# Performance work log

Hardware: AMD Instinct MI355X
Metric: run time of the kernel (lower is better)

The kernel has to match this reference:

```python
import jax, jax.numpy as jnp
import numpy as np

N = 524288   # number of (column, layer) samples
NCH = 30     # n_channel, fixed by the hard-coded filter vectors

# Per-gas channel filters for (h2o, o3, co2, u, n2o, ch4), each length 30.
FILTERS = jnp.array([
    [1,1,1,1,1,1,1,1,1,1,1,1,1,1,1,1,1,1,1,1,1,1,0,0,0,0,0,0,1,1],  # h2o
    [1,1,0,0,0,0,0,0,0,0,0,0,0,0,0,0,1,1,1,1,1,1,0,0,1,1,1,1,1,1],  # o3
    [1,1,0,0,1,1,0,0,1,1,0,0,1,1,0,0,0,0,0,0,0,0,0,0,0,0,0,0,1,1],  # co2
    [1,1,0,0,0,0,0,0,0,0,0,0,0,0,1,1,1,1,1,1,1,1,0,0,0,0,1,1,1,1],  # u
    [1,1,0,0,1,0,0,0,0,0,0,0,0,0,0,0,0,0,0,0,0,0,0,0,0,0,0,0,1,1],  # n2o
    [1,1,1,1,0,0,1,1,0,0,1,1,0,0,0,0,0,0,0,0,0,0,0,0,0,0,0,0,1,1],  # ch4
], dtype=jnp.float32)


def setup_inputs() -> dict:
    key = jax.random.key(0)
    ks = jax.random.split(key, 11)
    u = lambda k, shape, lo, hi: jax.random.uniform(k, shape, jnp.float32, lo, hi)
    return {
        "tpl": jax.random.normal(ks[0], (N, 3), jnp.float32),   # temp, pressure, log_pressure
        "cons": jax.random.uniform(ks[1], (N, 8), jnp.float32), # constituent masses
        # eight Linear(1, 30, bias=False) weights (lw, iw, h2o, o3, co2, u, n2o, ch4)
        "w_gas": u(ks[2], (8, NCH), -0.9, 0.5),
        # six ke-MLPs (2 -> 6 -> 4 -> 4 -> 1), stacked over gas axis g=6
        "ke_W1": u(ks[3], (6, 6, 2), -0.1, 0.1),
        "ke_b1": u(ks[4], (6, 6), 0.9, 1.1),
        "ke_W2": u(ks[5], (6, 4, 6), -0.1, 0.1),
        "ke_b2": u(ks[6], (6, 4), 0.9, 1.1),
        "ke_W3": u(ks[7], (6, 4, 4), -0.1, 0.1),
        "ke_b3": u(ks[8], (6, 4), 0.9, 1.1),
        "ke_Wo": u(ks[9], (6, 4), -0.1, 0.1),
        "ke_bo": u(ks[10], (6,), -0.1, 0.1),
    }


def reference(tpl, cons, w_gas, ke_W1, ke_b1, ke_W2, ke_b2, ke_W3, ke_b3, ke_Wo, ke_bo):
    t_p = tpl[:, :2]                                             # [N,2]
    # six tiny MLPs, vectorized over gas axis g (dropout is identity at eval)
    h = jax.nn.relu(jnp.einsum('ghi,ni->gnh', ke_W1, t_p) + ke_b1[:, None, :])   # [6,N,6]
    h = jax.nn.relu(jnp.einsum('goh,gnh->gno', ke_W2, h) + ke_b2[:, None, :])    # [6,N,4]
    h = jax.nn.relu(jnp.einsum('gph,gnh->gnp', ke_W3, h) + ke_b3[:, None, :])    # [6,N,4]
    s = jax.nn.sigmoid(jnp.einsum('gp,gnp->gn', ke_Wo, h) + ke_bo[:, None])      # [6,N]

    # net_gas(one) == weight vector; exp(w_gas) gives per-channel extinction coeffs
    tau_base = cons[:, None, :] * jnp.exp(w_gas).T[None, :, :]                   # [N,30,8]
    # channel filter * sigmoid modulation for the 6 gas species (slots 2..7)
    mod_gas = (FILTERS[:, None, :] * s[:, :, None]).transpose(1, 2, 0)           # [N,30,6]
    mod = jnp.concatenate(
        [jnp.ones((tpl.shape[0], NCH, 2), tau_base.dtype), mod_gas], axis=2)     # [N,30,8]
    return tau_base * mod                                                        # [N,30,8]
```

## Files before the change

kernel.cpp:

```cpp
#include <hip/hip_runtime.h>

#define NCHAN 30

__constant__ int FMASK_C[NCHAN] = {63,63,33,33,21,5,33,33,5,5,33,33,5,5,9,9,
                                   11,11,11,11,11,11,0,0,2,2,10,10,63,63};

typedef float f32x4 __attribute__((ext_vector_type(4)));

__global__ __launch_bounds__(256) void ext_kernel(
    const float* __restrict__ tpl,
    const float* __restrict__ cons,
    const float* __restrict__ w_gas,
    const float* __restrict__ W1, const float* __restrict__ b1,
    const float* __restrict__ W2, const float* __restrict__ b2,
    const float* __restrict__ W3, const float* __restrict__ b3,
    const float* __restrict__ Wo, const float* __restrict__ bo,
    f32x4* __restrict__ out4)
{
    __shared__ float p_lds[256][8];
    __shared__ float E_lds[32][8];

    const int tid = threadIdx.x;
    const int n   = blockIdx.x * 256 + tid;

    if (tid < 8 * NCHAN) {
        const int c = tid >> 3, k = tid & 7;
        float e = __expf(w_gas[k * NCHAN + c]);
        if (k >= 2 && !((FMASK_C[c] >> (k - 2)) & 1)) e = 0.f;
        E_lds[c][k] = e;
    }

    const float4* c4 = (const float4*)cons;
    const float4 ca = c4[(size_t)n * 2];
    const float4 cb = c4[(size_t)n * 2 + 1];
    const float t0 = tpl[(size_t)n * 3 + 0];
    const float t1 = tpl[(size_t)n * 3 + 1];

    float s[6];
    #pragma unroll
    for (int g = 0; g < 6; ++g) {
        float h1[6], h2[4], h3[4];
        #pragma unroll
        for (int j = 0; j < 6; ++j)
            h1[j] = fmaxf(0.f, fmaf(W1[g*12 + j*2], t0,
                           fmaf(W1[g*12 + j*2 + 1], t1, b1[g*6 + j])));
        #pragma unroll
        for (int o = 0; o < 4; ++o) {
            float a = b2[g*4 + o];
            #pragma unroll
            for (int j = 0; j < 6; ++j) a = fmaf(W2[g*24 + o*6 + j], h1[j], a);
            h2[o] = fmaxf(0.f, a);
        }
        #pragma unroll
        for (int p = 0; p < 4; ++p) {
            float a = b3[g*4 + p];
            #pragma unroll
            for (int o = 0; o < 4; ++o) a = fmaf(W3[g*16 + p*4 + o], h2[o], a);
            h3[p] = fmaxf(0.f, a);
        }
        float a = bo[g];
        #pragma unroll
        for (int p = 0; p < 4; ++p) a = fmaf(Wo[g*4 + p], h3[p], a);
        s[g] = __fdividef(1.f, 1.f + __expf(-a));
    }

    float4 pa, pb;
    pa.x = ca.x;        pa.y = ca.y;
    pa.z = ca.z * s[0]; pa.w = ca.w * s[1];
    pb.x = cb.x * s[2]; pb.y = cb.y * s[3];
    pb.z = cb.z * s[4]; pb.w = cb.w * s[5];
    *(float4*)&p_lds[tid][0] = pa;
    *(float4*)&p_lds[tid][4] = pb;

    __syncthreads();

    const int lane = tid & 63;
    const int wid  = tid >> 6;

    const int erem = (lane < 60) ? lane : 0;
    const float4 ev = *(const float4*)&E_lds[erem >> 1][(erem & 1) << 2];
    const unsigned hi4 = (unsigned)(lane & 1) << 2;

    const size_t gbase = (size_t)blockIdx.x * (256 * NCHAN * 2);

    if (lane < 60) {
        const int r0 = wid * 64;
        #pragma unroll 4
        for (int r = 0; r < 64; ++r) {
            const int nl = r0 + r;
            const float4 pv = *(const float4*)&p_lds[nl][hi4];

            f32x4 v;
            v.x = pv.x * ev.x;
            v.y = pv.y * ev.y;
            v.z = pv.z * ev.z;
            v.w = pv.w * ev.w;
            __builtin_nontemporal_store(v, &out4[gbase + (size_t)nl * 60 + lane]);
        }
    }
}

extern "C" void kernel_launch(void* const* d_in, const int* in_sizes, int n_in,
                              void* d_out, int out_size, void* d_ws, size_t ws_size,
                              hipStream_t stream) {
    const float* tpl  = (const float*)d_in[0];
    const float* cons = (const float*)d_in[1];
    const float* wgas = (const float*)d_in[2];
    const float* W1   = (const float*)d_in[3];
    const float* b1   = (const float*)d_in[4];
    const float* W2   = (const float*)d_in[5];
    const float* b2   = (const float*)d_in[6];
    const float* W3   = (const float*)d_in[7];
    const float* b3   = (const float*)d_in[8];
    const float* Wo   = (const float*)d_in[9];
    const float* bo   = (const float*)d_in[10];

    const int nrows  = in_sizes[0] / 3;
    const int blocks = nrows / 256;

    ext_kernel<<<dim3(blocks), dim3(256), 0, stream>>>(
        tpl, cons, wgas, W1, b1, W2, b2, W3, b3, Wo, bo, (f32x4*)d_out);
}
```

Measured before the change: 103.4 us.

## Make each wave process four row tiles with prefetch and wave-local LDS staging

Each wave now handles four consecutive 64-row tiles in a loop, using a per-wave LDS slice and wave barriers instead of a block-wide __syncthreads. The next tile's inputs are prefetched while the current tile's outputs are stored. The per-channel exp table is computed directly in registers per lane, which removes the shared E table and its block sync. Grid size shrinks by a factor of four, so per-block setup such as the exp work is amortised. The cost is fewer blocks to hide memory latency in a store-bound kernel.

Result: slower. 110.0 us (+6.3%).

```diff
diff --git a/kernel.cpp b/kernel.cpp
--- a/kernel.cpp
+++ b/kernel.cpp
@@ -1,6 +1,7 @@
 #include <hip/hip_runtime.h>
 
 #define NCHAN 30
+#define ITERS 4
 
 __constant__ int FMASK_C[NCHAN] = {63,63,33,33,21,5,33,33,5,5,33,33,5,5,9,9,
                                    11,11,11,11,11,11,0,0,2,2,10,10,63,63};
@@ -17,86 +18,99 @@
     const float* __restrict__ Wo, const float* __restrict__ bo,
     f32x4* __restrict__ out4)
 {
-    __shared__ float p_lds[256][8];
-    __shared__ float E_lds[32][8];
+    __shared__ float p_lds[4][64][8];
 
-    const int tid = threadIdx.x;
-    const int n   = blockIdx.x * 256 + tid;
-
-    if (tid < 8 * NCHAN) {
-        const int c = tid >> 3, k = tid & 7;
-        float e = __expf(w_gas[k * NCHAN + c]);
-        if (k >= 2 && !((FMASK_C[c] >> (k - 2)) & 1)) e = 0.f;
-        E_lds[c][k] = e;
-    }
-
-    const float4* c4 = (const float4*)cons;
-    const float4 ca = c4[(size_t)n * 2];
-    const float4 cb = c4[(size_t)n * 2 + 1];
-    const float t0 = tpl[(size_t)n * 3 + 0];
-    const float t1 = tpl[(size_t)n * 3 + 1];
-
-    float s[6];
-    #pragma unroll
-    for (int g = 0; g < 6; ++g) {
-        float h1[6], h2[4], h3[4];
-        #pragma unroll
-        for (int j = 0; j < 6; ++j)
-            h1[j] = fmaxf(0.f, fmaf(W1[g*12 + j*2], t0,
-                           fmaf(W1[g*12 + j*2 + 1], t1, b1[g*6 + j])));
-        #pragma unroll
-        for (int o = 0; o < 4; ++o) {
-            float a = b2[g*4 + o];
-            #pragma unroll
-            for (int j = 0; j < 6; ++j) a = fmaf(W2[g*24 + o*6 + j], h1[j], a);
-            h2[o] = fmaxf(0.f, a);
-        }
-        #pragma unroll
-        for (int p = 0; p < 4; ++p) {
-            float a = b3[g*4 + p];
-            #pragma unroll
-            for (int o = 0; o < 4; ++o) a = fmaf(W3[g*16 + p*4 + o], h2[o], a);
-            h3[p] = fmaxf(0.f, a);
-        }
-        float a = bo[g];
-        #pragma unroll
-        for (int p = 0; p < 4; ++p) a = fmaf(Wo[g*4 + p], h3[p], a);
-        s[g] = __fdividef(1.f, 1.f + __expf(-a));
-    }
-
-    float4 pa, pb;
-    pa.x = ca.x;        pa.y = ca.y;
-    pa.z = ca.z * s[0]; pa.w = ca.w * s[1];
-    pb.x = cb.x * s[2]; pb.y = cb.y * s[3];
-    pb.z = cb.z * s[4]; pb.w = cb.w * s[5];
-    *(float4*)&p_lds[tid][0] = pa;
-    *(float4*)&p_lds[tid][4] = pb;
-
-    __syncthreads();
-
+    const int tid  = threadIdx.x;
     const int lane = tid & 63;
     const int wid  = tid >> 6;
 
-    const int erem = (lane < 60) ? lane : 0;
-    const float4 ev = *(const float4*)&E_lds[erem >> 1][(erem & 1) << 2];
+    float4 ev;
+    {
+        const int rem = (lane < 60) ? lane : 0;
+        const int c  = rem >> 1;
+        const int k0 = (rem & 1) * 4;
+        float e[4];
+        #pragma unroll
+        for (int j = 0; j < 4; ++j) {
+            const int k = k0 + j;
+            float x = __expf(w_gas[k * NCHAN + c]);
+            if (k >= 2 && !((FMASK_C[c] >> (k - 2)) & 1)) x = 0.f;
+            e[j] = x;
+        }
+        ev.x = e[0]; ev.y = e[1]; ev.z = e[2]; ev.w = e[3];
+    }
     const unsigned hi4 = (unsigned)(lane & 1) << 2;
 
-    const size_t gbase = (size_t)blockIdx.x * (256 * NCHAN * 2);
+    const float4* c4 = (const float4*)cons;
+    const int wrow0 = blockIdx.x * (4 * 64 * ITERS) + wid * (64 * ITERS);
 
-    if (lane < 60) {
-        const int r0 = wid * 64;
-        #pragma unroll 4
-        for (int r = 0; r < 64; ++r) {
-            const int nl = r0 + r;
-            const float4 pv = *(const float4*)&p_lds[nl][hi4];
+    int row = wrow0 + lane;
+    float4 ca = c4[(size_t)row * 2];
+    float4 cb = c4[(size_t)row * 2 + 1];
+    float t0  = tpl[(size_t)row * 3 + 0];
+    float t1  = tpl[(size_t)row * 3 + 1];
 
-            f32x4 v;
-            v.x = pv.x * ev.x;
-            v.y = pv.y * ev.y;
-            v.z = pv.z * ev.z;
-            v.w = pv.w * ev.w;
-            __builtin_nontemporal_store(v, &out4[gbase + (size_t)nl * 60 + lane]);
+    for (int it = 0; it < ITERS; ++it) {
+        float s[6];
+        #pragma unroll
+        for (int g = 0; g < 6; ++g) {
+            float h1[6], h2[4], h3[4];
+            #pragma unroll
+            for (int j = 0; j < 6; ++j)
+                h1[j] = fmaxf(0.f, fmaf(W1[g*12 + j*2], t0,
+                               fmaf(W1[g*12 + j*2 + 1], t1, b1[g*6 + j])));
+            #pragma unroll
+            for (int o = 0; o < 4; ++o) {
+                float a = b2[g*4 + o];
+                #pragma unroll
+                for (int j = 0; j < 6; ++j) a = fmaf(W2[g*24 + o*6 + j], h1[j], a);
+                h2[o] = fmaxf(0.f, a);
+            }
+            #pragma unroll
+            for (int p = 0; p < 4; ++p) {
+                float a = b3[g*4 + p];
+                #pragma unroll
+                for (int o = 0; o < 4; ++o) a = fmaf(W3[g*16 + p*4 + o], h2[o], a);
+                h3[p] = fmaxf(0.f, a);
+            }
+            float a = bo[g];
+            #pragma unroll
+            for (int p = 0; p < 4; ++p) a = fmaf(Wo[g*4 + p], h3[p], a);
+            s[g] = __fdividef(1.f, 1.f + __expf(-a));
         }
+
+        float4 pa, pb;
+        pa.x = ca.x;        pa.y = ca.y;
+        pa.z = ca.z * s[0]; pa.w = ca.w * s[1];
+        pb.x = cb.x * s[2]; pb.y = cb.y * s[3];
+        pb.z = cb.z * s[4]; pb.w = cb.w * s[5];
+        *(float4*)&p_lds[wid][lane][0] = pa;
+        *(float4*)&p_lds[wid][lane][4] = pb;
+
+        __builtin_amdgcn_wave_barrier();
+
+        if (it + 1 < ITERS) {
+            const int nrow = wrow0 + (it + 1) * 64 + lane;
+            ca = c4[(size_t)nrow * 2];
+            cb = c4[(size_t)nrow * 2 + 1];
+            t0 = tpl[(size_t)nrow * 3 + 0];
+            t1 = tpl[(size_t)nrow * 3 + 1];
+        }
+
+        const size_t obase = (size_t)(wrow0 + it * 64) * (NCHAN * 2);
+        if (lane < 60) {
+            #pragma unroll 8
+            for (int r = 0; r < 64; ++r) {
+                const float4 pv = *(const float4*)&p_lds[wid][r][hi4];
+                f32x4 v;
+                v.x = pv.x * ev.x;
+                v.y = pv.y * ev.y;
+                v.z = pv.z * ev.z;
+                v.w = pv.w * ev.w;
+                __builtin_nontemporal_store(v, &out4[obase + (size_t)r * 60 + lane]);
+            }
+        }
+        __builtin_amdgcn_wave_barrier();
     }
 }
 
@@ -116,7 +130,7 @@
     const float* bo   = (const float*)d_in[10];
 
     const int nrows  = in_sizes[0] / 3;
-    const int blocks = nrows / 256;
+    const int blocks = nrows / (4 * 64 * ITERS);
 
     ext_kernel<<<dim3(blocks), dim3(256), 0, stream>>>(
         tpl, cons, wgas, W1, b1, W2, b2, W3, b3, Wo, bo, (f32x4*)d_out);
```
